# Optimization experiments

Measured on AMD Instinct MI355X. Metric: run time of the kernel, lower is better.

Reference implementation:

```python
import jax, jax.numpy as jnp
import numpy as np

N = 100000
E = 1600000
IN_DIM = 256
HID = 64


def setup_inputs() -> dict:
    key = jax.random.key(0)
    k1, k2, k3 = jax.random.split(key, 3)
    x = jax.random.normal(k1, (N, IN_DIM), dtype=jnp.float32)
    edge_index = jax.random.randint(k2, (2, E), 0, N, dtype=jnp.int64)
    # glorot-ish init for GCNConv weight, zero bias (PyG default)
    W = jax.random.normal(k3, (IN_DIM, HID), dtype=jnp.float32) * (1.0 / np.sqrt(IN_DIM))
    b = jnp.zeros((HID,), dtype=jnp.float32)
    return {"x": x, "edge_index": edge_index, "W": W, "b": b}


def reference(x, edge_index, W, b):
    # GCNConv: out = D^{-1/2} (A + I) D^{-1/2} (X W) + b
    n = x.shape[0]
    # add self-loops
    loop = jnp.arange(n, dtype=edge_index.dtype)
    src = jnp.concatenate([edge_index[0], loop])  # [E+N]
    dst = jnp.concatenate([edge_index[1], loop])  # [E+N]
    # degree of target nodes (incl. self-loops)
    deg = jax.ops.segment_sum(jnp.ones_like(dst, dtype=x.dtype), dst, num_segments=n)
    dinv = jnp.where(deg > 0, jax.lax.rsqrt(deg), 0.0)  # deg^{-1/2}, inf->0
    norm = dinv[src] * dinv[dst]  # [E+N]
    h = x @ W  # [N, HID] transform before aggregation
    msg = h[src] * norm[:, None]  # gather + scale, [E+N, HID]
    out = jax.ops.segment_sum(msg, dst, num_segments=n)  # scatter-add
    return out + b
```

## Files before the change

kernel.cpp:

```cpp
#include <hip/hip_runtime.h>

typedef float floatx4 __attribute__((ext_vector_type(4)));
typedef short s16x8 __attribute__((ext_vector_type(8)));

#define WG 256
#define NBUCK 512
#define BSH 8
#define EBLK 512
#define CAP 8192
#define MAXIT 16
#define CPAD 16

__device__ inline unsigned pack_bf16_rne(float a, float b) {
    unsigned ua = __float_as_uint(a), ub = __float_as_uint(b);
    ua = (ua + 0x7FFFu + ((ua >> 16) & 1u)) >> 16;
    ub = (ub + 0x7FFFu + ((ub >> 16) & 1u)) >> 16;
    return ua | (ub << 16);
}

union FragU {
    unsigned u[4];
    uint4 q;
    s16x8 v;
};

__global__ __launch_bounds__(WG) void k_packw(const float* __restrict__ W,
                                              uint4* __restrict__ wpack,
                                              int* __restrict__ cursor) {
    const int q = blockIdx.x * WG + threadIdx.x;
    for (int z = q; z < NBUCK * CPAD; z += 2048) cursor[z] = 0;
    const int kb = q >> 8, nt = (q >> 6) & 3, ln = q & 63;
    const int quad = ln >> 4, l15 = ln & 15;
    const int col = nt * 16 + l15;
    const int krow = kb * 32 + quad * 8;
    unsigned up[4];
#pragma unroll
    for (int p = 0; p < 4; p++) {
        float a = W[(krow + 2 * p) * 64 + col];
        float b2 = W[(krow + 2 * p + 1) * 64 + col];
        up[p] = pack_bf16_rne(a, b2);
    }
    uint4 pk = {up[0], up[1], up[2], up[3]};
    wpack[q] = pk;
}

__global__ __launch_bounds__(WG, 4) void k_main(const void* __restrict__ ei, int* __restrict__ cursor,
                                                unsigned* __restrict__ ebuf, int E,
                                                const float* __restrict__ x, const uint4* __restrict__ wpack,
                                                unsigned short* __restrict__ g, int N) {
    __shared__ int hh[NBUCK];
    __shared__ int hbase[NBUCK];
    __shared__ int s32flag;
    const int t = threadIdx.x;

    if ((int)blockIdx.x < EBLK) {
        if (t == 0) s32flag = 0;
        for (int i = t; i < NBUCK; i += WG) hh[i] = 0;
        __syncthreads();
        {
            const int* w = (const int*)ei;
            int nz = 0;
            for (int j = t; j < 4096; j += WG) nz |= (w[2 * j + 1] != 0);
            if (nz) atomicOr(&s32flag, 1);
        }
        __syncthreads();
        const bool i32 = (s32flag != 0);
        const int chunk = (E + EBLK - 1) / EBLK;
        const int s = blockIdx.x * chunk;
        const int eend = min(E, s + chunk);

        if (chunk <= MAXIT * WG) {
            unsigned ew[MAXIT];
            unsigned short ebk[MAXIT];
#pragma unroll
            for (int i = 0; i < MAXIT; i++) {
                const int e = s + t + i * WG;
                ebk[i] = 0xFFFFu;
                if (e < eend) {
                    int sN, dN;
                    if (i32) {
                        const int* p = (const int*)ei;
                        sN = p[e];
                        dN = p[E + e];
                    } else {
                        const long long* p = (const long long*)ei;
                        sN = (int)p[e];
                        dN = (int)p[(long long)E + e];
                    }
                    ew[i] = (unsigned)sN | ((unsigned)(dN & 255) << 24);
                    ebk[i] = (unsigned short)(dN >> BSH);
                    atomicAdd(&hh[dN >> BSH], 1);
                }
            }
            __syncthreads();
            for (int i = t; i < NBUCK; i += WG) {
                int c = hh[i];
                hbase[i] = c ? atomicAdd(&cursor[i * CPAD], c) : 0;
                hh[i] = 0;
            }
            __syncthreads();
#pragma unroll
            for (int i = 0; i < MAXIT; i++) {
                if (ebk[i] != 0xFFFFu) {
                    const int bkt = ebk[i];
                    const int pos = hbase[bkt] + atomicAdd(&hh[bkt], 1);
                    if (pos < CAP) ebuf[(size_t)bkt * CAP + pos] = ew[i];
                }
            }
        } else {
            if (i32) {
                const int* pd = (const int*)ei + E;
                for (int e = s + t; e < eend; e += WG) atomicAdd(&hh[pd[e] >> BSH], 1);
            } else {
                const long long* pd = (const long long*)ei + E;
                for (int e = s + t; e < eend; e += WG) atomicAdd(&hh[(int)pd[e] >> BSH], 1);
            }
            __syncthreads();
            for (int i = t; i < NBUCK; i += WG) {
                int c = hh[i];
                hbase[i] = c ? atomicAdd(&cursor[i * CPAD], c) : 0;
                hh[i] = 0;
            }
            __syncthreads();
            for (int e = s + t; e < eend; e += WG) {
                int sN, dN;
                if (i32) {
                    const int* p = (const int*)ei;
                    sN = p[e];
                    dN = p[E + e];
                } else {
                    const long long* p = (const long long*)ei;
                    sN = (int)p[e];
                    dN = (int)p[(long long)E + e];
                }
                int bkt = dN >> BSH;
                int pos = hbase[bkt] + atomicAdd(&hh[bkt], 1);
                if (pos < CAP) ebuf[(size_t)bkt * CAP + pos] = (unsigned)sN | ((unsigned)(dN & 255) << 24);
            }
        }
    } else {
        const int bb = blockIdx.x - EBLK;
        const int wv = t >> 6;
        const int lane = t & 63;
        const int quad = lane >> 4, l15 = lane & 15;

        long long arow = (long long)bb * 64 + wv * 16 + l15;
        if (arow >= N) arow = N - 1;
        const float* xr = x + arow * 256 + quad * 8;
        const uint4* wp = wpack + lane;

        floatx4 xv[8][2];
#pragma unroll
        for (int kb = 0; kb < 8; kb++) {
            const float* p = xr + kb * 32;
            asm volatile("global_load_dwordx4 %0, %2, off\n\t"
                         "global_load_dwordx4 %1, %2, off offset:16"
                         : "=&v"(xv[kb][0]), "=&v"(xv[kb][1])
                         : "v"(p));
        }
        asm volatile("s_waitcnt vmcnt(0)"
                     : "+v"(xv[0][0]), "+v"(xv[0][1]), "+v"(xv[1][0]), "+v"(xv[1][1]),
                       "+v"(xv[2][0]), "+v"(xv[2][1]), "+v"(xv[3][0]), "+v"(xv[3][1]),
                       "+v"(xv[4][0]), "+v"(xv[4][1]), "+v"(xv[5][0]), "+v"(xv[5][1]),
                       "+v"(xv[6][0]), "+v"(xv[6][1]), "+v"(xv[7][0]), "+v"(xv[7][1]));
        __builtin_amdgcn_sched_barrier(0);

        floatx4 acc[4];
#pragma unroll
        for (int nt = 0; nt < 4; nt++) acc[nt] = 0.f;

        FragU bc0, bc1, bc2, bc3;
        bc0.q = wp[0 * 64];
        bc1.q = wp[1 * 64];
        bc2.q = wp[2 * 64];
        bc3.q = wp[3 * 64];

#pragma unroll
        for (int kb = 0; kb < 8; kb++) {
            FragU bn0, bn1, bn2, bn3;
            if (kb < 7) {
                bn0.q = wp[((kb + 1) * 4 + 0) * 64];
                bn1.q = wp[((kb + 1) * 4 + 1) * 64];
                bn2.q = wp[((kb + 1) * 4 + 2) * 64];
                bn3.q = wp[((kb + 1) * 4 + 3) * 64];
            }
            FragU a;
            a.u[0] = pack_bf16_rne(xv[kb][0][0], xv[kb][0][1]);
            a.u[1] = pack_bf16_rne(xv[kb][0][2], xv[kb][0][3]);
            a.u[2] = pack_bf16_rne(xv[kb][1][0], xv[kb][1][1]);
            a.u[3] = pack_bf16_rne(xv[kb][1][2], xv[kb][1][3]);
            acc[0] = __builtin_amdgcn_mfma_f32_16x16x32_bf16(a.v, bc0.v, acc[0], 0, 0, 0);
            acc[1] = __builtin_amdgcn_mfma_f32_16x16x32_bf16(a.v, bc1.v, acc[1], 0, 0, 0);
            acc[2] = __builtin_amdgcn_mfma_f32_16x16x32_bf16(a.v, bc2.v, acc[2], 0, 0, 0);
            acc[3] = __builtin_amdgcn_mfma_f32_16x16x32_bf16(a.v, bc3.v, acc[3], 0, 0, 0);
            if (kb < 7) {
                bc0 = bn0;
                bc1 = bn1;
                bc2 = bn2;
                bc3 = bn3;
            }
        }

        const long long orow0 = (long long)bb * 64 + wv * 16 + quad * 4;
#pragma unroll
        for (int r = 0; r < 4; r++) {
            const long long orow = orow0 + r;
            if (orow < N) {
#pragma unroll
                for (int nt = 0; nt < 4; nt++) {
                    float v = acc[nt][r];
                    unsigned uv = __float_as_uint(v);
                    uv = (uv + 0x7FFFu + ((uv >> 16) & 1u)) >> 16;
                    g[orow * 64 + nt * 16 + l15] = (unsigned short)uv;
                }
            }
        }
    }
}

__global__ __launch_bounds__(WG) void k_csr(const unsigned* __restrict__ ebuf, const int* __restrict__ cursor,
                                            int* __restrict__ off, int* __restrict__ srcs,
                                            float* __restrict__ dinv, int N, int nbuse) {
    __shared__ int red[256];
    __shared__ int h[256];
    __shared__ int sc[256];
    __shared__ int cur[256];
    const int t = threadIdx.x;
    const int b = blockIdx.x;
    const int node0 = b << BSH;
    const int rows = min(256, N - node0);
    int part = 0;
    for (int i = t; i < b; i += WG) part += min(cursor[i * CPAD], CAP);
    red[t] = part;
    h[t] = 0;
    __syncthreads();
    for (int d = WG / 2; d > 0; d >>= 1) {
        if (t < d) red[t] += red[t + d];
        __syncthreads();
    }
    const int ebase = red[0];
    const int cnt = min(cursor[b * CPAD], CAP);
    const unsigned* eb = ebuf + (size_t)b * CAP;
    for (int j = t; j < cnt; j += WG) atomicAdd(&h[eb[j] >> 24], 1);
    __syncthreads();
    const int deg = (t < rows) ? h[t] + 1 : 0;
    sc[t] = deg;
    __syncthreads();
    for (int d = 1; d < 256; d <<= 1) {
        int a = (t >= d) ? sc[t - d] : 0;
        __syncthreads();
        sc[t] += a;
        __syncthreads();
    }
    const int basef = ebase + node0;
    const int local = sc[t] - deg;
    if (t < rows) {
        off[node0 + t] = basef + local;
        srcs[basef + local] = node0 + t;
        cur[t] = local + 1;
        dinv[node0 + t] = rsqrtf((float)deg);
    }
    if (b == nbuse - 1 && t == 0) off[N] = ebase + cnt + N;
    __syncthreads();
    for (int j = t; j < cnt; j += WG) {
        unsigned w = eb[j];
        int dl = (int)(w >> 24);
        int pos = basef + atomicAdd(&cur[dl], 1);
        srcs[pos] = (int)(w & 0xFFFFFFu);
    }
}

__global__ __launch_bounds__(WG) void k_gather(const unsigned short* __restrict__ g,
                                               const int* __restrict__ off, const int* __restrict__ srcs,
                                               const float* __restrict__ dinv, const float* __restrict__ bias,
                                               float* __restrict__ out, int N) {
    const int t = threadIdx.x;
    const int node = blockIdx.x * 32 + (t >> 3);
    if (node >= N) return;
    const int c8 = (t & 7) * 8;
    const int e1 = off[node + 1];
    int e = off[node];
    float a0 = 0.f, a1 = 0.f, a2 = 0.f, a3 = 0.f, a4 = 0.f, a5 = 0.f, a6 = 0.f, a7 = 0.f;
    int s = srcs[e];
    while (e < e1) {
        const int en = e + 1;
        const int sn = (en < e1) ? srcs[en] : 0;
        const float ds = dinv[s];
        const uint4 v = *(const uint4*)(g + (long long)s * 64 + c8);
        a0 += ds * __uint_as_float(v.x << 16);
        a1 += ds * __uint_as_float(v.x & 0xFFFF0000u);
        a2 += ds * __uint_as_float(v.y << 16);
        a3 += ds * __uint_as_float(v.y & 0xFFFF0000u);
        a4 += ds * __uint_as_float(v.z << 16);
        a5 += ds * __uint_as_float(v.z & 0xFFFF0000u);
        a6 += ds * __uint_as_float(v.w << 16);
        a7 += ds * __uint_as_float(v.w & 0xFFFF0000u);
        s = sn;
        e = en;
    }
    const float d = dinv[node];
    const floatx4 b0 = *(const floatx4*)(bias + c8);
    const floatx4 b1 = *(const floatx4*)(bias + c8 + 4);
    floatx4 o0, o1;
    o0[0] = d * a0 + b0[0];
    o0[1] = d * a1 + b0[1];
    o0[2] = d * a2 + b0[2];
    o0[3] = d * a3 + b0[3];
    o1[0] = d * a4 + b1[0];
    o1[1] = d * a5 + b1[1];
    o1[2] = d * a6 + b1[2];
    o1[3] = d * a7 + b1[3];
    *(floatx4*)(out + (long long)node * 64 + c8) = o0;
    *(floatx4*)(out + (long long)node * 64 + c8 + 4) = o1;
}

extern "C" void kernel_launch(void* const* d_in, const int* in_sizes, int n_in,
                              void* d_out, int out_size, void* d_ws, size_t ws_size,
                              hipStream_t stream) {
    const float* x = (const float*)d_in[0];
    const void* ei = d_in[1];
    const float* W = (const float*)d_in[2];
    const float* b = (const float*)d_in[3];
    float* out = (float*)d_out;

    const int N = in_sizes[0] / 256;
    const int E = in_sizes[1] / 2;
    const int NBUSE = (N + 255) >> BSH;
    const int GEMMB = (N + 63) / 64;

    char* ws = (char*)d_ws;
    size_t o = 0;
    auto alloc = [&](size_t bytes) -> void* {
        void* p = ws + o;
        o += (bytes + 255) & ~(size_t)255;
        return p;
    };
    float* dinv = (float*)alloc((size_t)N * 4);
    unsigned short* g = (unsigned short*)alloc((size_t)N * 64 * 2);
    unsigned* ebuf = (unsigned*)alloc((size_t)NBUSE * CAP * 4);
    int* cursor = (int*)alloc((size_t)NBUCK * CPAD * 4);
    int* off = (int*)alloc((size_t)(N + 1) * 4);
    int* srcs = (int*)alloc((size_t)(E + N) * 4);
    uint4* wpack = (uint4*)alloc((size_t)2048 * 16);
    if (o > ws_size) return;

    k_packw<<<8, WG, 0, stream>>>(W, wpack, cursor);
    k_main<<<EBLK + GEMMB, WG, 0, stream>>>(ei, cursor, ebuf, E, x, wpack, g, N);
    k_csr<<<NBUSE, WG, 0, stream>>>(ebuf, cursor, off, srcs, dinv, N, NBUSE);
    k_gather<<<(N + 31) / 32, WG, 0, stream>>>(g, off, srcs, dinv, b, out, N);
}
```

Before: 258.3 us.

## Replace CSR build and gather with per-bucket shared-memory scatter accumulation

Result: slower. 926.2 us (+258.6%).

```diff
diff --git a/kernel.cpp b/kernel.cpp
--- a/kernel.cpp
+++ b/kernel.cpp
@@ -4,10 +4,10 @@
 typedef short s16x8 __attribute__((ext_vector_type(8)));
 
 #define WG 256
-#define NBUCK 512
-#define BSH 8
+#define NBUCK 1024
+#define BSH 7
 #define EBLK 512
-#define CAP 8192
+#define CAP 4096
 #define MAXIT 16
 #define CPAD 16
 
@@ -24,28 +24,32 @@
     s16x8 v;
 };
 
-__global__ __launch_bounds__(WG) void k_packw(const float* __restrict__ W,
-                                              uint4* __restrict__ wpack,
-                                              int* __restrict__ cursor) {
+__global__ __launch_bounds__(WG) void k_init(const float* __restrict__ W,
+                                             uint4* __restrict__ wpack,
+                                             int* __restrict__ cursor,
+                                             int* __restrict__ deg, int N) {
     const int q = blockIdx.x * WG + threadIdx.x;
-    for (int z = q; z < NBUCK * CPAD; z += 2048) cursor[z] = 0;
-    const int kb = q >> 8, nt = (q >> 6) & 3, ln = q & 63;
-    const int quad = ln >> 4, l15 = ln & 15;
-    const int col = nt * 16 + l15;
-    const int krow = kb * 32 + quad * 8;
-    unsigned up[4];
-#pragma unroll
-    for (int p = 0; p < 4; p++) {
-        float a = W[(krow + 2 * p) * 64 + col];
-        float b2 = W[(krow + 2 * p + 1) * 64 + col];
-        up[p] = pack_bf16_rne(a, b2);
-    }
-    uint4 pk = {up[0], up[1], up[2], up[3]};
-    wpack[q] = pk;
+    for (int z = q; z < NBUCK * CPAD; z += 32768) cursor[z] = 0;
+    for (int z = q; z < N; z += 32768) deg[z] = 0;
+    if (q < 2048) {
+        const int kb = q >> 8, nt = (q >> 6) & 3, ln = q & 63;
+        const int quad = ln >> 4, l15 = ln & 15;
+        const int col = nt * 16 + l15;
+        const int krow = kb * 32 + quad * 8;
+        unsigned up[4];
+#pragma unroll
+        for (int p = 0; p < 4; p++) {
+            float a = W[(krow + 2 * p) * 64 + col];
+            float b2 = W[(krow + 2 * p + 1) * 64 + col];
+            up[p] = pack_bf16_rne(a, b2);
+        }
+        uint4 pk = {up[0], up[1], up[2], up[3]};
+        wpack[q] = pk;
+    }
 }
 
 __global__ __launch_bounds__(WG, 4) void k_main(const void* __restrict__ ei, int* __restrict__ cursor,
-                                                unsigned* __restrict__ ebuf, int E,
+                                                unsigned* __restrict__ ebuf, int* __restrict__ deg, int E,
                                                 const float* __restrict__ x, const uint4* __restrict__ wpack,
                                                 unsigned short* __restrict__ g, int N) {
     __shared__ int hh[NBUCK];
@@ -87,9 +91,10 @@
                         sN = (int)p[e];
                         dN = (int)p[(long long)E + e];
                     }
-                    ew[i] = (unsigned)sN | ((unsigned)(dN & 255) << 24);
+                    ew[i] = (unsigned)sN | ((unsigned)(dN & 127) << 24);
                     ebk[i] = (unsigned short)(dN >> BSH);
                     atomicAdd(&hh[dN >> BSH], 1);
+                    atomicAdd(&deg[dN], 1);
                 }
             }
             __syncthreads();
@@ -110,10 +115,18 @@
         } else {
             if (i32) {
                 const int* pd = (const int*)ei + E;
-                for (int e = s + t; e < eend; e += WG) atomicAdd(&hh[pd[e] >> BSH], 1);
+                for (int e = s + t; e < eend; e += WG) {
+                    const int dN = pd[e];
+                    atomicAdd(&hh[dN >> BSH], 1);
+                    atomicAdd(&deg[dN], 1);
+                }
             } else {
                 const long long* pd = (const long long*)ei + E;
-                for (int e = s + t; e < eend; e += WG) atomicAdd(&hh[(int)pd[e] >> BSH], 1);
+                for (int e = s + t; e < eend; e += WG) {
+                    const int dN = (int)pd[e];
+                    atomicAdd(&hh[dN >> BSH], 1);
+                    atomicAdd(&deg[dN], 1);
+                }
             }
             __syncthreads();
             for (int i = t; i < NBUCK; i += WG) {
@@ -135,7 +148,7 @@
                 }
                 int bkt = dN >> BSH;
                 int pos = hbase[bkt] + atomicAdd(&hh[bkt], 1);
-                if (pos < CAP) ebuf[(size_t)bkt * CAP + pos] = (unsigned)sN | ((unsigned)(dN & 255) << 24);
+                if (pos < CAP) ebuf[(size_t)bkt * CAP + pos] = (unsigned)sN | ((unsigned)(dN & 127) << 24);
             }
         }
     } else {
@@ -148,6 +161,13 @@
         if (arow >= N) arow = N - 1;
         const float* xr = x + arow * 256 + quad * 8;
         const uint4* wp = wpack + lane;
+
+        FragU bc0, bc1, bc2, bc3;
+        bc0.q = wp[0 * 64];
+        bc1.q = wp[1 * 64];
+        bc2.q = wp[2 * 64];
+        bc3.q = wp[3 * 64];
+        __builtin_amdgcn_sched_barrier(0);
 
         floatx4 xv[8][2];
 #pragma unroll
@@ -168,12 +188,6 @@
         floatx4 acc[4];
 #pragma unroll
         for (int nt = 0; nt < 4; nt++) acc[nt] = 0.f;
-
-        FragU bc0, bc1, bc2, bc3;
-        bc0.q = wp[0 * 64];
-        bc1.q = wp[1 * 64];
-        bc2.q = wp[2 * 64];
-        bc3.q = wp[3 * 64];
 
 #pragma unroll
         for (int kb = 0; kb < 8; kb++) {
@@ -218,100 +232,100 @@
     }
 }
 
-__global__ __launch_bounds__(WG) void k_csr(const unsigned* __restrict__ ebuf, const int* __restrict__ cursor,
-                                            int* __restrict__ off, int* __restrict__ srcs,
-                                            float* __restrict__ dinv, int N, int nbuse) {
-    __shared__ int red[256];
-    __shared__ int h[256];
-    __shared__ int sc[256];
-    __shared__ int cur[256];
+__global__ __launch_bounds__(WG) void k_acc(const unsigned* __restrict__ ebuf, const int* __restrict__ cursor,
+                                            const int* __restrict__ deg, const unsigned short* __restrict__ g,
+                                            const float* __restrict__ bias, float* __restrict__ out, int N) {
+    __shared__ float acc[128][64];
     const int t = threadIdx.x;
     const int b = blockIdx.x;
     const int node0 = b << BSH;
-    const int rows = min(256, N - node0);
-    int part = 0;
-    for (int i = t; i < b; i += WG) part += min(cursor[i * CPAD], CAP);
-    red[t] = part;
-    h[t] = 0;
+    const int grp = t >> 3;
+    const int c0 = (t & 7) * 8;
+
+#pragma unroll
+    for (int it = 0; it < 4; it++) {
+        const int dl = it * 32 + grp;
+        const int node = node0 + dl;
+        if (node < N) {
+            const float ds = rsqrtf((float)(deg[node] + 1));
+            const uint4 v = *(const uint4*)(g + (size_t)node * 64 + c0);
+            float* ar = acc[dl];
+            ar[(c0 + 0 + dl) & 63] = ds * __uint_as_float(v.x << 16);
+            ar[(c0 + 1 + dl) & 63] = ds * __uint_as_float(v.x & 0xFFFF0000u);
+            ar[(c0 + 2 + dl) & 63] = ds * __uint_as_float(v.y << 16);
+            ar[(c0 + 3 + dl) & 63] = ds * __uint_as_float(v.y & 0xFFFF0000u);
+            ar[(c0 + 4 + dl) & 63] = ds * __uint_as_float(v.z << 16);
+            ar[(c0 + 5 + dl) & 63] = ds * __uint_as_float(v.z & 0xFFFF0000u);
+            ar[(c0 + 6 + dl) & 63] = ds * __uint_as_float(v.w << 16);
+            ar[(c0 + 7 + dl) & 63] = ds * __uint_as_float(v.w & 0xFFFF0000u);
+        }
+    }
     __syncthreads();
-    for (int d = WG / 2; d > 0; d >>= 1) {
-        if (t < d) red[t] += red[t + d];
-        __syncthreads();
-    }
-    const int ebase = red[0];
+
     const int cnt = min(cursor[b * CPAD], CAP);
     const unsigned* eb = ebuf + (size_t)b * CAP;
-    for (int j = t; j < cnt; j += WG) atomicAdd(&h[eb[j] >> 24], 1);
+    int j = grp;
+    unsigned ew0 = 0, ew1 = 0;
+    int dg0 = 0;
+    uint4 v0 = {0, 0, 0, 0};
+    if (j < cnt) {
+        ew0 = eb[j];
+        const int s0 = (int)(ew0 & 0xFFFFFFu);
+        dg0 = deg[s0];
+        v0 = *(const uint4*)(g + (size_t)s0 * 64 + c0);
+    }
+    if (j + 32 < cnt) ew1 = eb[j + 32];
+    while (j < cnt) {
+        unsigned ew2 = 0;
+        int dg1 = 0;
+        uint4 v1 = v0;
+        if (j + 32 < cnt) {
+            const int s1 = (int)(ew1 & 0xFFFFFFu);
+            dg1 = deg[s1];
+            v1 = *(const uint4*)(g + (size_t)s1 * 64 + c0);
+        }
+        if (j + 64 < cnt) ew2 = eb[j + 64];
+        const int dl = (int)(ew0 >> 24);
+        const float ds = rsqrtf((float)(dg0 + 1));
+        float* ar = acc[dl];
+        atomicAdd(&ar[(c0 + 0 + dl) & 63], ds * __uint_as_float(v0.x << 16));
+        atomicAdd(&ar[(c0 + 1 + dl) & 63], ds * __uint_as_float(v0.x & 0xFFFF0000u));
+        atomicAdd(&ar[(c0 + 2 + dl) & 63], ds * __uint_as_float(v0.y << 16));
+        atomicAdd(&ar[(c0 + 3 + dl) & 63], ds * __uint_as_float(v0.y & 0xFFFF0000u));
+        atomicAdd(&ar[(c0 + 4 + dl) & 63], ds * __uint_as_float(v0.z << 16));
+        atomicAdd(&ar[(c0 + 5 + dl) & 63], ds * __uint_as_float(v0.z & 0xFFFF0000u));
+        atomicAdd(&ar[(c0 + 6 + dl) & 63], ds * __uint_as_float(v0.w << 16));
+        atomicAdd(&ar[(c0 + 7 + dl) & 63], ds * __uint_as_float(v0.w & 0xFFFF0000u));
+        ew0 = ew1;
+        ew1 = ew2;
+        dg0 = dg1;
+        v0 = v1;
+        j += 32;
+    }
     __syncthreads();
-    const int deg = (t < rows) ? h[t] + 1 : 0;
-    sc[t] = deg;
-    __syncthreads();
-    for (int d = 1; d < 256; d <<= 1) {
-        int a = (t >= d) ? sc[t - d] : 0;
-        __syncthreads();
-        sc[t] += a;
-        __syncthreads();
-    }
-    const int basef = ebase + node0;
-    const int local = sc[t] - deg;
-    if (t < rows) {
-        off[node0 + t] = basef + local;
-        srcs[basef + local] = node0 + t;
-        cur[t] = local + 1;
-        dinv[node0 + t] = rsqrtf((float)deg);
-    }
-    if (b == nbuse - 1 && t == 0) off[N] = ebase + cnt + N;
-    __syncthreads();
-    for (int j = t; j < cnt; j += WG) {
-        unsigned w = eb[j];
-        int dl = (int)(w >> 24);
-        int pos = basef + atomicAdd(&cur[dl], 1);
-        srcs[pos] = (int)(w & 0xFFFFFFu);
-    }
-}
-
-__global__ __launch_bounds__(WG) void k_gather(const unsigned short* __restrict__ g,
-                                               const int* __restrict__ off, const int* __restrict__ srcs,
-                                               const float* __restrict__ dinv, const float* __restrict__ bias,
-                                               float* __restrict__ out, int N) {
-    const int t = threadIdx.x;
-    const int node = blockIdx.x * 32 + (t >> 3);
-    if (node >= N) return;
-    const int c8 = (t & 7) * 8;
-    const int e1 = off[node + 1];
-    int e = off[node];
-    float a0 = 0.f, a1 = 0.f, a2 = 0.f, a3 = 0.f, a4 = 0.f, a5 = 0.f, a6 = 0.f, a7 = 0.f;
-    int s = srcs[e];
-    while (e < e1) {
-        const int en = e + 1;
-        const int sn = (en < e1) ? srcs[en] : 0;
-        const float ds = dinv[s];
-        const uint4 v = *(const uint4*)(g + (long long)s * 64 + c8);
-        a0 += ds * __uint_as_float(v.x << 16);
-        a1 += ds * __uint_as_float(v.x & 0xFFFF0000u);
-        a2 += ds * __uint_as_float(v.y << 16);
-        a3 += ds * __uint_as_float(v.y & 0xFFFF0000u);
-        a4 += ds * __uint_as_float(v.z << 16);
-        a5 += ds * __uint_as_float(v.z & 0xFFFF0000u);
-        a6 += ds * __uint_as_float(v.w << 16);
-        a7 += ds * __uint_as_float(v.w & 0xFFFF0000u);
-        s = sn;
-        e = en;
-    }
-    const float d = dinv[node];
-    const floatx4 b0 = *(const floatx4*)(bias + c8);
-    const floatx4 b1 = *(const floatx4*)(bias + c8 + 4);
-    floatx4 o0, o1;
-    o0[0] = d * a0 + b0[0];
-    o0[1] = d * a1 + b0[1];
-    o0[2] = d * a2 + b0[2];
-    o0[3] = d * a3 + b0[3];
-    o1[0] = d * a4 + b1[0];
-    o1[1] = d * a5 + b1[1];
-    o1[2] = d * a6 + b1[2];
-    o1[3] = d * a7 + b1[3];
-    *(floatx4*)(out + (long long)node * 64 + c8) = o0;
-    *(floatx4*)(out + (long long)node * 64 + c8 + 4) = o1;
+
+#pragma unroll
+    for (int it = 0; it < 4; it++) {
+        const int dl = it * 32 + grp;
+        const int node = node0 + dl;
+        if (node < N) {
+            const float dsd = rsqrtf((float)(deg[node] + 1));
+            const float* ar = acc[dl];
+            const floatx4 b0 = *(const floatx4*)(bias + c0);
+            const floatx4 b1 = *(const floatx4*)(bias + c0 + 4);
+            floatx4 o0, o1;
+            o0[0] = dsd * ar[(c0 + 0 + dl) & 63] + b0[0];
+            o0[1] = dsd * ar[(c0 + 1 + dl) & 63] + b0[1];
+            o0[2] = dsd * ar[(c0 + 2 + dl) & 63] + b0[2];
+            o0[3] = dsd * ar[(c0 + 3 + dl) & 63] + b0[3];
+            o1[0] = dsd * ar[(c0 + 4 + dl) & 63] + b1[0];
+            o1[1] = dsd * ar[(c0 + 5 + dl) & 63] + b1[1];
+            o1[2] = dsd * ar[(c0 + 6 + dl) & 63] + b1[2];
+            o1[3] = dsd * ar[(c0 + 7 + dl) & 63] + b1[3];
+            *(floatx4*)(out + (size_t)node * 64 + c0) = o0;
+            *(floatx4*)(out + (size_t)node * 64 + c0 + 4) = o1;
+        }
+    }
 }
 
 extern "C" void kernel_launch(void* const* d_in, const int* in_sizes, int n_in,
@@ -325,7 +339,7 @@
 
     const int N = in_sizes[0] / 256;
     const int E = in_sizes[1] / 2;
-    const int NBUSE = (N + 255) >> BSH;
+    const int NBUSE = (N + 127) >> BSH;
     const int GEMMB = (N + 63) / 64;
 
     char* ws = (char*)d_ws;
@@ -335,17 +349,14 @@
         o += (bytes + 255) & ~(size_t)255;
         return p;
     };
-    float* dinv = (float*)alloc((size_t)N * 4);
     unsigned short* g = (unsigned short*)alloc((size_t)N * 64 * 2);
-    unsigned* ebuf = (unsigned*)alloc((size_t)NBUSE * CAP * 4);
+    unsigned* ebuf = (unsigned*)alloc((size_t)NBUCK * CAP * 4);
     int* cursor = (int*)alloc((size_t)NBUCK * CPAD * 4);
-    int* off = (int*)alloc((size_t)(N + 1) * 4);
-    int* srcs = (int*)alloc((size_t)(E + N) * 4);
+    int* deg = (int*)alloc((size_t)N * 4);
     uint4* wpack = (uint4*)alloc((size_t)2048 * 16);
     if (o > ws_size) return;
 
-    k_packw<<<8, WG, 0, stream>>>(W, wpack, cursor);
-    k_main<<<EBLK + GEMMB, WG, 0, stream>>>(ei, cursor, ebuf, E, x, wpack, g, N);
-    k_csr<<<NBUSE, WG, 0, stream>>>(ebuf, cursor, off, srcs, dinv, N, NBUSE);
-    k_gather<<<(N + 31) / 32, WG, 0, stream>>>(g, off, srcs, dinv, b, out, N);
-}
+    k_init<<<128, WG, 0, stream>>>(W, wpack, cursor, deg, N);
+    k_main<<<EBLK + GEMMB, WG, 0, stream>>>(ei, cursor, ebuf, deg, E, x, wpack, g, N);
+    k_acc<<<NBUSE, WG, 0, stream>>>(ebuf, cursor, deg, g, b, out, N);
+}
```
